# Kernel optimization log

Measured on AMD Instinct MI355X. Metric: run time of the kernel, lower is better.

The kernel has to match this reference:

```python
import jax, jax.numpy as jnp
import numpy as np

N, E = 40000, 640000
S_IN, V_IN = 64, 32            # input irreps: 64x0e + 32x1o (dim 160)
S_MID, V_MID = 96, 128         # tp output: (64+32)x0e, (64+32+32)x1o
S_OUT, V_OUT = 96, 32          # gate irreps_in: 64x0e scalars + 32x0e gates + 32x1o gated
R = 64                         # edge scalar (radial basis) dim
FC_HID = 64
W_NUMEL = 64 + 64 + 32 + 32 + 32  # per-edge tp weights ('uvu', v=1): 224
NUM_NEIGHBORS = 16.0


def setup_inputs() -> dict:
    key = jax.random.key(0)
    ks = jax.random.split(key, 13)
    return {
        "node_features": jax.random.normal(ks[0], (N, S_IN + 3 * V_IN), jnp.float32),
        "node_attr": jnp.ones((N, 1), jnp.float32),
        "edge_src": jax.random.randint(ks[1], (E,), 0, N),
        "edge_dst": jax.random.randint(ks[2], (E,), 0, N),
        "edge_attr": jax.random.normal(ks[3], (E, 4), jnp.float32),
        "edge_scalars": jax.random.normal(ks[4], (E, R), jnp.float32),
        "lin1_ws": jax.random.normal(ks[5], (S_IN, S_IN), jnp.float32),
        "lin1_wv": jax.random.normal(ks[6], (V_IN, V_IN), jnp.float32),
        "fc_w1": jax.random.normal(ks[7], (R, FC_HID), jnp.float32),
        "fc_w2": jax.random.normal(ks[8], (FC_HID, W_NUMEL), jnp.float32),
        "sc_ws": jax.random.normal(ks[9], (S_IN, S_OUT), jnp.float32),
        "sc_wv": jax.random.normal(ks[10], (V_IN, V_OUT), jnp.float32),
        "lin2_ws": jax.random.normal(ks[11], (S_MID, S_OUT), jnp.float32),
        "lin2_wv": jax.random.normal(ks[12], (V_MID, V_OUT), jnp.float32),
    }


def _inv(d):
    return 1.0 / jnp.sqrt(jnp.float32(d))


def _forward(node_features, node_attr, edge_attr, edge_scalars,
             lin1_ws, lin1_wv, fc_w1, fc_w2, sc_ws, sc_wv, lin2_ws, lin2_wv,
             edge_src, edge_dst):
    n = node_features.shape[0]
    s = node_features[:, :S_IN]                      # [N,64] 0e
    v = node_features[:, S_IN:].reshape(n, V_IN, 3)  # [N,32,3] 1o
    a = node_attr                                    # [N,1] scalar node attr

    # self-connection: FullyConnectedTensorProduct(input, 1x0e attr, out) == per-irrep linear
    sc_s = (s @ sc_ws) * a * _inv(S_IN)                                    # [N,96]
    sc_v = jnp.einsum('nci,cd->ndi', v, sc_wv) * a[:, :, None] * _inv(V_IN)  # [N,32,3]

    # lin1
    h_s = (s @ lin1_ws) * a * _inv(S_IN)
    h_v = jnp.einsum('nci,cd->ndi', v, lin1_wv) * a[:, :, None] * _inv(V_IN)

    # per-edge tensor-product weights from FC on edge scalars (silu MLP, no bias)
    hid = jax.nn.silu((edge_scalars @ fc_w1) * _inv(R))
    w = (hid @ fc_w2) * _inv(FC_HID)                 # [E,224]
    w1, w2, w3, w4, w5 = jnp.split(w, [64, 128, 160, 192], axis=-1)

    # gather source node features
    es = h_s[edge_src]                               # [E,64]
    ev = h_v[edge_src]                               # [E,32,3]
    e0 = edge_attr[:, :1]                            # [E,1]  0e
    e1 = edge_attr[:, 1:4]                           # [E,3]  1o

    # Clebsch-Gordan tensor product paths ('uvu', per-edge weights)
    m_s1 = w1 * es * e0                                                   # 0e x 0e -> 0e [E,64]
    m_s2 = w4 * jnp.einsum('eci,ei->ec', ev, e1) * _inv(3)                # 1o x 1o -> 0e [E,32]
    m_v1 = (w2 * es)[:, :, None] * e1[:, None, :]                         # 0e x 1o -> 1o [E,64,3]
    m_v2 = w3[:, :, None] * ev * e0[:, :, None]                           # 1o x 0e -> 1o [E,32,3]
    m_v3 = w5[:, :, None] * jnp.cross(ev, e1[:, None, :]) * _inv(2)       # 1o x 1o -> 1o [E,32,3]

    mid_s = jnp.concatenate([m_s1, m_s2], axis=-1)        # [E,96]
    mid_v = jnp.concatenate([m_v1, m_v2, m_v3], axis=1)   # [E,128,3]

    # scatter-sum to destination nodes, normalized by sqrt(num_neighbors)
    inv_nn = 1.0 / jnp.sqrt(jnp.float32(NUM_NEIGHBORS))
    agg_s = jax.ops.segment_sum(mid_s, edge_dst, num_segments=n) * inv_nn
    agg_v = jax.ops.segment_sum(mid_v, edge_dst, num_segments=n) * inv_nn

    # lin2
    o_s = (agg_s @ lin2_ws) * a * _inv(S_MID)                                  # [N,96]
    o_v = jnp.einsum('nci,cd->ndi', agg_v, lin2_wv) * a[:, :, None] * _inv(V_MID)  # [N,32,3]

    pre_s = sc_s + o_s
    pre_v = sc_v + o_v

    # Gate: silu on scalars, sigmoid gates multiply the l=1 features
    scalars = jax.nn.silu(pre_s[:, :64])
    gates = jax.nn.sigmoid(pre_s[:, 64:96])
    gated = gates[:, :, None] * pre_v                 # [N,32,3]
    return jnp.concatenate([scalars, gated.reshape(n, 3 * V_OUT)], axis=-1)  # [N,160]


def reference(node_features, node_attr, edge_src, edge_dst, edge_attr, edge_scalars,
              lin1_ws, lin1_wv, fc_w1, fc_w2, sc_ws, sc_wv, lin2_ws, lin2_wv):
    return _forward(node_features, node_attr, edge_attr, edge_scalars,
                    lin1_ws, lin1_wv, fc_w1, fc_w2, sc_ws, sc_wv, lin2_ws, lin2_wv,
                    edge_src, edge_dst)
```

## Files before the change

### kernel.cpp

```cpp
#include <hip/hip_runtime.h>

constexpr int N_NODES = 40000;
constexpr int N_EDGES = 640000;

constexpr float C_INV8     = 0.125f;
constexpr float C_INV_S32  = 0.17677669529663687f;
constexpr float C_INV_S3   = 0.57735026918962576f;
constexpr float C_INV_S2   = 0.70710678118654752f;
constexpr float C_INV_S96  = 0.10206207261596575f;
constexpr float C_INV_S128 = 0.08838834764831845f;
constexpr float C_INV_NN   = 0.25f;

typedef __attribute__((ext_vector_type(8))) short short8;
typedef __attribute__((ext_vector_type(4))) float f32x4;

__device__ __forceinline__ unsigned short f2bf(float x) {
  union { float f; unsigned int u; } v; v.f = x;
  unsigned int r = v.u + 0x7fffu + ((v.u >> 16) & 1u);
  return (unsigned short)(r >> 16);
}
__device__ __forceinline__ float bf2f(unsigned short h) {
  return __uint_as_float(((unsigned int)h) << 16);
}

__global__ __launch_bounds__(256) void k_prep(
    const float* __restrict__ fc_w1, const float* __restrict__ fc_w2,
    const float* __restrict__ lin2_ws, const float* __restrict__ lin2_wv,
    unsigned short* __restrict__ w1t, unsigned short* __restrict__ w2t,
    unsigned short* __restrict__ wst, unsigned short* __restrict__ wvt)
{
  int t = blockIdx.x * 256 + threadIdx.x;
  if (t < 4096) {
    int c = t >> 6, k = t & 63;
    w1t[c * 64 + k] = f2bf(fc_w1[k * 64 + c]);
  } else if (t < 4096 + 14336) {
    int u = t - 4096; int c = u >> 6, k = u & 63;
    w2t[c * 64 + k] = f2bf(fc_w2[k * 224 + c]);
  } else if (t < 18432 + 9216) {
    int u = t - 18432; int c = u / 96, k = u - c * 96;
    wst[c * 96 + k] = f2bf(lin2_ws[k * 96 + c]);
  } else if (t < 27648 + 4096) {
    int u = t - 27648; int d = u >> 7, k = u & 127;
    wvt[d * 128 + k] = f2bf(lin2_wv[k * 32 + d]);
  }
}

__global__ __launch_bounds__(256) void k_node_hs(
    const float* __restrict__ nf, const float* __restrict__ attr,
    const float* __restrict__ w, float* __restrict__ h_s)
{
  int t = blockIdx.x * 256 + threadIdx.x;
  if (t >= N_NODES * 64) return;
  int n = t >> 6, c = t & 63;
  const float* s = nf + (long)n * 160;
  float acc = 0.f;
  #pragma unroll 8
  for (int k = 0; k < 64; ++k) acc = fmaf(s[k], w[k * 64 + c], acc);
  h_s[t] = acc * attr[n] * C_INV8;
}

__global__ __launch_bounds__(256) void k_node_hv(
    const float* __restrict__ nf, const float* __restrict__ attr,
    const float* __restrict__ w, float* __restrict__ h_v)
{
  int t = blockIdx.x * 256 + threadIdx.x;
  if (t >= N_NODES * 32) return;
  int n = t >> 5, d = t & 31;
  const float* v = nf + (long)n * 160 + 64;
  float a0 = 0.f, a1 = 0.f, a2 = 0.f;
  #pragma unroll 8
  for (int c = 0; c < 32; ++c) {
    float wv = w[c * 32 + d];
    a0 = fmaf(v[3 * c + 0], wv, a0);
    a1 = fmaf(v[3 * c + 1], wv, a1);
    a2 = fmaf(v[3 * c + 2], wv, a2);
  }
  float sc = attr[n] * C_INV_S32;
  h_v[(long)t * 3 + 0] = a0 * sc;
  h_v[(long)t * 3 + 1] = a1 * sc;
  h_v[(long)t * 3 + 2] = a2 * sc;
}

__global__ __launch_bounds__(256, 2) void k_edge(
    const float* __restrict__ escal, const float* __restrict__ eattr,
    const int* __restrict__ esrc, const int* __restrict__ edst,
    const unsigned short* __restrict__ w1t, const unsigned short* __restrict__ w2t,
    const unsigned short* __restrict__ wst, const unsigned short* __restrict__ wvt,
    const float* __restrict__ h_s, const float* __restrict__ h_v,
    float* __restrict__ agg_s, float* __restrict__ agg_v)
{
  __shared__ unsigned short hid_lds[64 * 72];
  __shared__ unsigned short w_lds[64 * 232];
  int tid = threadIdx.x, warp = tid >> 6, lane = tid & 63;
  int lr = lane & 15, lg = lane >> 4;
  long e0 = (long)blockIdx.x * 64;
  int r0 = warp * 16;

  f32x4 acc[4] = {};
  #pragma unroll
  for (int ks = 0; ks < 2; ++ks) {
    const float* ap = escal + (e0 + r0 + lr) * 64 + ks * 32 + lg * 8;
    float4 a01 = *reinterpret_cast<const float4*>(ap);
    float4 a23 = *reinterpret_cast<const float4*>(ap + 4);
    short8 af;
    af[0] = (short)f2bf(a01.x); af[1] = (short)f2bf(a01.y);
    af[2] = (short)f2bf(a01.z); af[3] = (short)f2bf(a01.w);
    af[4] = (short)f2bf(a23.x); af[5] = (short)f2bf(a23.y);
    af[6] = (short)f2bf(a23.z); af[7] = (short)f2bf(a23.w);
    #pragma unroll
    for (int nt = 0; nt < 4; ++nt) {
      short8 bf = *reinterpret_cast<const short8*>(w1t + (nt * 16 + lr) * 64 + ks * 32 + lg * 8);
      acc[nt] = __builtin_amdgcn_mfma_f32_16x16x32_bf16(af, bf, acc[nt], 0, 0, 0);
    }
  }
  #pragma unroll
  for (int nt = 0; nt < 4; ++nt)
    #pragma unroll
    for (int r = 0; r < 4; ++r) {
      float x = acc[nt][r] * C_INV8;
      float h = x / (1.f + __expf(-x));
      hid_lds[(r0 + lg * 4 + r) * 72 + nt * 16 + lr] = f2bf(h);
    }
  __syncthreads();

  f32x4 acc2[14] = {};
  #pragma unroll
  for (int ks = 0; ks < 2; ++ks) {
    short8 af = *reinterpret_cast<const short8*>(hid_lds + (r0 + lr) * 72 + ks * 32 + lg * 8);
    #pragma unroll
    for (int nt = 0; nt < 14; ++nt) {
      short8 bf = *reinterpret_cast<const short8*>(w2t + (nt * 16 + lr) * 64 + ks * 32 + lg * 8);
      acc2[nt] = __builtin_amdgcn_mfma_f32_16x16x32_bf16(af, bf, acc2[nt], 0, 0, 0);
    }
  }
  #pragma unroll
  for (int nt = 0; nt < 14; ++nt)
    #pragma unroll
    for (int r = 0; r < 4; ++r)
      w_lds[(r0 + lg * 4 + r) * 232 + nt * 16 + lr] = f2bf(acc2[nt][r] * C_INV8);
  __syncthreads();

  long eM = e0 + r0 + lr;
  int srcM = esrc[eM];
  float ea0 = eattr[eM * 4 + 0];
  float e1x = eattr[eM * 4 + 1], e1y = eattr[eM * 4 + 2], e1z = eattr[eM * 4 + 3];

  float esv[16];
  {
    const float* hsr = h_s + (long)srcM * 64;
    *reinterpret_cast<float4*>(&esv[0])  = *reinterpret_cast<const float4*>(hsr + lg * 8);
    *reinterpret_cast<float4*>(&esv[4])  = *reinterpret_cast<const float4*>(hsr + lg * 8 + 4);
    *reinterpret_cast<float4*>(&esv[8])  = *reinterpret_cast<const float4*>(hsr + 32 + lg * 8);
    *reinterpret_cast<float4*>(&esv[12]) = *reinterpret_cast<const float4*>(hsr + 32 + lg * 8 + 4);
  }
  float evv[24];
  {
    const float* hvr = h_v + (long)srcM * 96 + lg * 24;
    #pragma unroll
    for (int q = 0; q < 6; ++q)
      *reinterpret_cast<float4*>(&evv[4 * q]) = *reinterpret_cast<const float4*>(hvr + 4 * q);
  }
  const unsigned short* wrow = w_lds + (r0 + lr) * 232;
  short8 w1a = *reinterpret_cast<const short8*>(wrow + lg * 8);
  short8 w1b = *reinterpret_cast<const short8*>(wrow + 32 + lg * 8);
  short8 w2a = *reinterpret_cast<const short8*>(wrow + 64 + lg * 8);
  short8 w2b = *reinterpret_cast<const short8*>(wrow + 96 + lg * 8);
  short8 w3s = *reinterpret_cast<const short8*>(wrow + 128 + lg * 8);
  short8 w4s = *reinterpret_cast<const short8*>(wrow + 160 + lg * 8);
  short8 w5s = *reinterpret_cast<const short8*>(wrow + 192 + lg * 8);

  f32x4 accS[6] = {};
  {
    short8 aS;
    #pragma unroll
    for (int j = 0; j < 8; ++j) aS[j] = (short)f2bf(bf2f((unsigned short)w1a[j]) * esv[j] * ea0);
    #pragma unroll
    for (int nt = 0; nt < 6; ++nt) {
      short8 b = *reinterpret_cast<const short8*>(wst + (nt * 16 + lr) * 96 + lg * 8);
      accS[nt] = __builtin_amdgcn_mfma_f32_16x16x32_bf16(aS, b, accS[nt], 0, 0, 0);
    }
    #pragma unroll
    for (int j = 0; j < 8; ++j) aS[j] = (short)f2bf(bf2f((unsigned short)w1b[j]) * esv[8 + j] * ea0);
    #pragma unroll
    for (int nt = 0; nt < 6; ++nt) {
      short8 b = *reinterpret_cast<const short8*>(wst + (nt * 16 + lr) * 96 + 32 + lg * 8);
      accS[nt] = __builtin_amdgcn_mfma_f32_16x16x32_bf16(aS, b, accS[nt], 0, 0, 0);
    }
    #pragma unroll
    for (int j = 0; j < 8; ++j) {
      float dot = evv[3 * j] * e1x + evv[3 * j + 1] * e1y + evv[3 * j + 2] * e1z;
      aS[j] = (short)f2bf(bf2f((unsigned short)w4s[j]) * dot * C_INV_S3);
    }
    #pragma unroll
    for (int nt = 0; nt < 6; ++nt) {
      short8 b = *reinterpret_cast<const short8*>(wst + (nt * 16 + lr) * 96 + 64 + lg * 8);
      accS[nt] = __builtin_amdgcn_mfma_f32_16x16x32_bf16(aS, b, accS[nt], 0, 0, 0);
    }
  }

  f32x4 accV[6] = {};
  #pragma unroll
  for (int i = 0; i < 3; ++i) {
    float e1i = (i == 0) ? e1x : (i == 1) ? e1y : e1z;
    short8 aV;
    #pragma unroll
    for (int j = 0; j < 8; ++j) aV[j] = (short)f2bf(bf2f((unsigned short)w2a[j]) * esv[j] * e1i);
    #pragma unroll
    for (int nt = 0; nt < 2; ++nt) {
      short8 b = *reinterpret_cast<const short8*>(wvt + (nt * 16 + lr) * 128 + lg * 8);
      accV[i * 2 + nt] = __builtin_amdgcn_mfma_f32_16x16x32_bf16(aV, b, accV[i * 2 + nt], 0, 0, 0);
    }
    #pragma unroll
    for (int j = 0; j < 8; ++j) aV[j] = (short)f2bf(bf2f((unsigned short)w2b[j]) * esv[8 + j] * e1i);
    #pragma unroll
    for (int nt = 0; nt < 2; ++nt) {
      short8 b = *reinterpret_cast<const short8*>(wvt + (nt * 16 + lr) * 128 + 32 + lg * 8);
      accV[i * 2 + nt] = __builtin_amdgcn_mfma_f32_16x16x32_bf16(aV, b, accV[i * 2 + nt], 0, 0, 0);
    }
    #pragma unroll
    for (int j = 0; j < 8; ++j) aV[j] = (short)f2bf(bf2f((unsigned short)w3s[j]) * evv[3 * j + i] * ea0);
    #pragma unroll
    for (int nt = 0; nt < 2; ++nt) {
      short8 b = *reinterpret_cast<const short8*>(wvt + (nt * 16 + lr) * 128 + 64 + lg * 8);
      accV[i * 2 + nt] = __builtin_amdgcn_mfma_f32_16x16x32_bf16(aV, b, accV[i * 2 + nt], 0, 0, 0);
    }
    #pragma unroll
    for (int j = 0; j < 8; ++j) {
      float ex = evv[3 * j], ey = evv[3 * j + 1], ez = evv[3 * j + 2];
      float cr = (i == 0) ? (ey * e1z - ez * e1y)
               : (i == 1) ? (ez * e1x - ex * e1z)
                          : (ex * e1y - ey * e1x);
      aV[j] = (short)f2bf(bf2f((unsigned short)w5s[j]) * cr * C_INV_S2);
    }
    #pragma unroll
    for (int nt = 0; nt < 2; ++nt) {
      short8 b = *reinterpret_cast<const short8*>(wvt + (nt * 16 + lr) * 128 + 96 + lg * 8);
      accV[i * 2 + nt] = __builtin_amdgcn_mfma_f32_16x16x32_bf16(aV, b, accV[i * 2 + nt], 0, 0, 0);
    }
  }

  #pragma unroll
  for (int r = 0; r < 4; ++r) {
    int dstR = edst[e0 + r0 + lg * 4 + r];
    float* asp = agg_s + (long)dstR * 96;
    #pragma unroll
    for (int nt = 0; nt < 6; ++nt) unsafeAtomicAdd(&asp[nt * 16 + lr], accS[nt][r]);
    float* avp = agg_v + (long)dstR * 96;
    #pragma unroll
    for (int q = 0; q < 6; ++q) {
      int i = q >> 1, nt = q & 1;
      unsafeAtomicAdd(&avp[i * 32 + nt * 16 + lr], accV[q][r]);
    }
  }
}

__global__ __launch_bounds__(256) void k_fin_s(
    const float* __restrict__ nf, const float* __restrict__ attr,
    const float* __restrict__ agg_s, const float* __restrict__ sc_ws,
    float* __restrict__ out, float* __restrict__ gate)
{
  int t = blockIdx.x * 256 + threadIdx.x;
  if (t >= N_NODES * 96) return;
  int n = t / 96, cch = t - n * 96;
  const float* s = nf + (long)n * 160;
  float acc2 = 0.f;
  #pragma unroll 8
  for (int k = 0; k < 64; ++k) acc2 = fmaf(s[k], sc_ws[k * 96 + cch], acc2);
  float pre = (agg_s[t] * (C_INV_NN * C_INV_S96) + acc2 * C_INV8) * attr[n];
  if (cch < 64) out[(long)n * 160 + cch] = pre / (1.f + __expf(-pre));
  else gate[n * 32 + cch - 64] = 1.f / (1.f + __expf(-pre));
}

__global__ __launch_bounds__(256) void k_fin_v(
    const float* __restrict__ nf, const float* __restrict__ attr,
    const float* __restrict__ agg_v, const float* __restrict__ sc_wv,
    const float* __restrict__ gate, float* __restrict__ out)
{
  int t = blockIdx.x * 256 + threadIdx.x;
  if (t >= N_NODES * 32) return;
  int n = t >> 5, d = t & 31;
  const float* v = nf + (long)n * 160 + 64;
  float s0 = 0.f, s1 = 0.f, s2 = 0.f;
  #pragma unroll 8
  for (int cc = 0; cc < 32; ++cc) {
    float wv = sc_wv[cc * 32 + d];
    s0 = fmaf(v[3 * cc + 0], wv, s0);
    s1 = fmaf(v[3 * cc + 1], wv, s1);
    s2 = fmaf(v[3 * cc + 2], wv, s2);
  }
  const float* ag = agg_v + (long)n * 96;
  float a = attr[n];
  float g = gate[t];
  float p0 = (ag[0 * 32 + d] * (C_INV_NN * C_INV_S128) + s0 * C_INV_S32) * a;
  float p1 = (ag[1 * 32 + d] * (C_INV_NN * C_INV_S128) + s1 * C_INV_S32) * a;
  float p2 = (ag[2 * 32 + d] * (C_INV_NN * C_INV_S128) + s2 * C_INV_S32) * a;
  float* o = out + (long)n * 160 + 64 + 3 * d;
  o[0] = g * p0; o[1] = g * p1; o[2] = g * p2;
}

extern "C" void kernel_launch(void* const* d_in, const int* in_sizes, int n_in,
                              void* d_out, int out_size, void* d_ws, size_t ws_size,
                              hipStream_t stream)
{
  const float* nf      = (const float*)d_in[0];
  const float* attr    = (const float*)d_in[1];
  const int*   esrc    = (const int*)d_in[2];
  const int*   edst    = (const int*)d_in[3];
  const float* eattr   = (const float*)d_in[4];
  const float* escal   = (const float*)d_in[5];
  const float* lin1_ws = (const float*)d_in[6];
  const float* lin1_wv = (const float*)d_in[7];
  const float* fc_w1   = (const float*)d_in[8];
  const float* fc_w2   = (const float*)d_in[9];
  const float* sc_ws   = (const float*)d_in[10];
  const float* sc_wv   = (const float*)d_in[11];
  const float* lin2_ws = (const float*)d_in[12];
  const float* lin2_wv = (const float*)d_in[13];
  float* out = (float*)d_out;

  float* ws    = (float*)d_ws;
  float* h_s   = ws;
  float* h_v   = h_s + (size_t)N_NODES * 64;
  float* agg_s = h_v + (size_t)N_NODES * 96;
  float* agg_v = agg_s + (size_t)N_NODES * 96;
  unsigned short* w1t = (unsigned short*)(agg_v + (size_t)N_NODES * 96);
  unsigned short* w2t = w1t + 64 * 64;
  unsigned short* wst = w2t + 224 * 64;
  unsigned short* wvt = wst + 96 * 96;
  float* gate = h_s;

  hipMemsetAsync(agg_s, 0, (size_t)N_NODES * 192 * sizeof(float), stream);
  k_prep<<<124, 256, 0, stream>>>(fc_w1, fc_w2, lin2_ws, lin2_wv, w1t, w2t, wst, wvt);
  k_node_hs<<<(N_NODES * 64 + 255) / 256, 256, 0, stream>>>(nf, attr, lin1_ws, h_s);
  k_node_hv<<<(N_NODES * 32 + 255) / 256, 256, 0, stream>>>(nf, attr, lin1_wv, h_v);
  k_edge<<<N_EDGES / 64, 256, 0, stream>>>(escal, eattr, esrc, edst,
                                           w1t, w2t, wst, wvt, h_s, h_v, agg_s, agg_v);
  k_fin_s<<<(N_NODES * 96 + 255) / 256, 256, 0, stream>>>(nf, attr, agg_s, sc_ws, out, gate);
  k_fin_v<<<(N_NODES * 32 + 255) / 256, 256, 0, stream>>>(nf, attr, agg_v, sc_wv, gate, out);
}
```

Before: 614.3 us.

## Replace atomic scatter with CSR-sorted gather aggregation of bf16 edge outputs

```diff
diff --git a/kernel.cpp b/kernel.cpp
--- a/kernel.cpp
+++ b/kernel.cpp
@@ -81,13 +81,64 @@
   h_v[(long)t * 3 + 2] = a2 * sc;
 }
 
-__global__ __launch_bounds__(256, 2) void k_edge(
+__global__ __launch_bounds__(256) void k_deg(const int* __restrict__ edst,
+                                             int* __restrict__ deg)
+{
+  int e = blockIdx.x * 256 + threadIdx.x;
+  if (e < N_EDGES) atomicAdd(&deg[edst[e]], 1);
+}
+
+__global__ __launch_bounds__(1024) void k_scan(const int* __restrict__ deg,
+                                               int* __restrict__ start,
+                                               int* __restrict__ cursor)
+{
+  __shared__ int psum[1024];
+  int tid = threadIdx.x;
+  const int PER = 40;
+  int base = tid * PER;
+  int s = 0;
+  for (int i = 0; i < PER; ++i) {
+    int idx = base + i;
+    if (idx < N_NODES) s += deg[idx];
+  }
+  psum[tid] = s;
+  __syncthreads();
+  for (int off = 1; off < 1024; off <<= 1) {
+    int v = psum[tid];
+    int u = (tid >= off) ? psum[tid - off] : 0;
+    __syncthreads();
+    psum[tid] = v + u;
+    __syncthreads();
+  }
+  int run = (tid == 0) ? 0 : psum[tid - 1];
+  for (int i = 0; i < PER; ++i) {
+    int idx = base + i;
+    if (idx < N_NODES) {
+      start[idx] = run; cursor[idx] = run;
+      run += deg[idx];
+    }
+  }
+  if (tid == 1023) start[N_NODES] = run;
+}
+
+__global__ __launch_bounds__(256) void k_fill(const int* __restrict__ edst,
+                                              int* __restrict__ cursor,
+                                              int* __restrict__ eid)
+{
+  int e = blockIdx.x * 256 + threadIdx.x;
+  if (e < N_EDGES) {
+    int p = atomicAdd(&cursor[edst[e]], 1);
+    eid[p] = e;
+  }
+}
+
+__global__ __launch_bounds__(256, 2) void k_edge2(
     const float* __restrict__ escal, const float* __restrict__ eattr,
-    const int* __restrict__ esrc, const int* __restrict__ edst,
+    const int* __restrict__ esrc,
     const unsigned short* __restrict__ w1t, const unsigned short* __restrict__ w2t,
     const unsigned short* __restrict__ wst, const unsigned short* __restrict__ wvt,
     const float* __restrict__ h_s, const float* __restrict__ h_v,
-    float* __restrict__ agg_s, float* __restrict__ agg_v)
+    unsigned short* __restrict__ e_out)
 {
   __shared__ unsigned short hid_lds[64 * 72];
   __shared__ unsigned short w_lds[64 * 232];
@@ -239,24 +290,217 @@
     }
   }
 
+  __syncthreads();
+  unsigned short* o_lds = w_lds;
+  #pragma unroll
+  for (int nt = 0; nt < 6; ++nt)
+    #pragma unroll
+    for (int r = 0; r < 4; ++r)
+      o_lds[(r0 + lg * 4 + r) * 200 + nt * 16 + lr] = f2bf(accS[nt][r]);
+  #pragma unroll
+  for (int q = 0; q < 6; ++q) {
+    int i = q >> 1, nt = q & 1;
+    #pragma unroll
+    for (int r = 0; r < 4; ++r)
+      o_lds[(r0 + lg * 4 + r) * 200 + 96 + i * 32 + nt * 16 + lr] = f2bf(accV[q][r]);
+  }
+  __syncthreads();
+
+  int row = tid >> 2, quad = tid & 3;
+  #pragma unroll
+  for (int c6 = 0; c6 < 6; ++c6) {
+    int cb = quad * 48 + c6 * 8;
+    float4 v4 = *reinterpret_cast<const float4*>(o_lds + row * 200 + cb);
+    *reinterpret_cast<float4*>(e_out + (e0 + row) * 192 + cb) = v4;
+  }
+}
+
+__global__ __launch_bounds__(256, 2) void k_edge_at(
+    const float* __restrict__ escal, const float* __restrict__ eattr,
+    const int* __restrict__ esrc, const int* __restrict__ edst,
+    const unsigned short* __restrict__ w1t, const unsigned short* __restrict__ w2t,
+    const unsigned short* __restrict__ wst, const unsigned short* __restrict__ wvt,
+    const float* __restrict__ h_s, const float* __restrict__ h_v,
+    float* __restrict__ agg)
+{
+  __shared__ unsigned short hid_lds[64 * 72];
+  __shared__ unsigned short w_lds[64 * 232];
+  int tid = threadIdx.x, warp = tid >> 6, lane = tid & 63;
+  int lr = lane & 15, lg = lane >> 4;
+  long e0 = (long)blockIdx.x * 64;
+  int r0 = warp * 16;
+
+  f32x4 acc[4] = {};
+  #pragma unroll
+  for (int ks = 0; ks < 2; ++ks) {
+    const float* ap = escal + (e0 + r0 + lr) * 64 + ks * 32 + lg * 8;
+    float4 a01 = *reinterpret_cast<const float4*>(ap);
+    float4 a23 = *reinterpret_cast<const float4*>(ap + 4);
+    short8 af;
+    af[0] = (short)f2bf(a01.x); af[1] = (short)f2bf(a01.y);
+    af[2] = (short)f2bf(a01.z); af[3] = (short)f2bf(a01.w);
+    af[4] = (short)f2bf(a23.x); af[5] = (short)f2bf(a23.y);
+    af[6] = (short)f2bf(a23.z); af[7] = (short)f2bf(a23.w);
+    #pragma unroll
+    for (int nt = 0; nt < 4; ++nt) {
+      short8 bf = *reinterpret_cast<const short8*>(w1t + (nt * 16 + lr) * 64 + ks * 32 + lg * 8);
+      acc[nt] = __builtin_amdgcn_mfma_f32_16x16x32_bf16(af, bf, acc[nt], 0, 0, 0);
+    }
+  }
+  #pragma unroll
+  for (int nt = 0; nt < 4; ++nt)
+    #pragma unroll
+    for (int r = 0; r < 4; ++r) {
+      float x = acc[nt][r] * C_INV8;
+      float h = x / (1.f + __expf(-x));
+      hid_lds[(r0 + lg * 4 + r) * 72 + nt * 16 + lr] = f2bf(h);
+    }
+  __syncthreads();
+
+  f32x4 acc2[14] = {};
+  #pragma unroll
+  for (int ks = 0; ks < 2; ++ks) {
+    short8 af = *reinterpret_cast<const short8*>(hid_lds + (r0 + lr) * 72 + ks * 32 + lg * 8);
+    #pragma unroll
+    for (int nt = 0; nt < 14; ++nt) {
+      short8 bf = *reinterpret_cast<const short8*>(w2t + (nt * 16 + lr) * 64 + ks * 32 + lg * 8);
+      acc2[nt] = __builtin_amdgcn_mfma_f32_16x16x32_bf16(af, bf, acc2[nt], 0, 0, 0);
+    }
+  }
+  #pragma unroll
+  for (int nt = 0; nt < 14; ++nt)
+    #pragma unroll
+    for (int r = 0; r < 4; ++r)
+      w_lds[(r0 + lg * 4 + r) * 232 + nt * 16 + lr] = f2bf(acc2[nt][r] * C_INV8);
+  __syncthreads();
+
+  long eM = e0 + r0 + lr;
+  int srcM = esrc[eM];
+  float ea0 = eattr[eM * 4 + 0];
+  float e1x = eattr[eM * 4 + 1], e1y = eattr[eM * 4 + 2], e1z = eattr[eM * 4 + 3];
+  float esv[16];
+  {
+    const float* hsr = h_s + (long)srcM * 64;
+    *reinterpret_cast<float4*>(&esv[0])  = *reinterpret_cast<const float4*>(hsr + lg * 8);
+    *reinterpret_cast<float4*>(&esv[4])  = *reinterpret_cast<const float4*>(hsr + lg * 8 + 4);
+    *reinterpret_cast<float4*>(&esv[8])  = *reinterpret_cast<const float4*>(hsr + 32 + lg * 8);
+    *reinterpret_cast<float4*>(&esv[12]) = *reinterpret_cast<const float4*>(hsr + 32 + lg * 8 + 4);
+  }
+  float evv[24];
+  {
+    const float* hvr = h_v + (long)srcM * 96 + lg * 24;
+    #pragma unroll
+    for (int q = 0; q < 6; ++q)
+      *reinterpret_cast<float4*>(&evv[4 * q]) = *reinterpret_cast<const float4*>(hvr + 4 * q);
+  }
+  const unsigned short* wrow = w_lds + (r0 + lr) * 232;
+  short8 w1a = *reinterpret_cast<const short8*>(wrow + lg * 8);
+  short8 w1b = *reinterpret_cast<const short8*>(wrow + 32 + lg * 8);
+  short8 w2a = *reinterpret_cast<const short8*>(wrow + 64 + lg * 8);
+  short8 w2b = *reinterpret_cast<const short8*>(wrow + 96 + lg * 8);
+  short8 w3s = *reinterpret_cast<const short8*>(wrow + 128 + lg * 8);
+  short8 w4s = *reinterpret_cast<const short8*>(wrow + 160 + lg * 8);
+  short8 w5s = *reinterpret_cast<const short8*>(wrow + 192 + lg * 8);
+
+  f32x4 accS[6] = {};
+  {
+    short8 aS;
+    #pragma unroll
+    for (int j = 0; j < 8; ++j) aS[j] = (short)f2bf(bf2f((unsigned short)w1a[j]) * esv[j] * ea0);
+    #pragma unroll
+    for (int nt = 0; nt < 6; ++nt) {
+      short8 b = *reinterpret_cast<const short8*>(wst + (nt * 16 + lr) * 96 + lg * 8);
+      accS[nt] = __builtin_amdgcn_mfma_f32_16x16x32_bf16(aS, b, accS[nt], 0, 0, 0);
+    }
+    #pragma unroll
+    for (int j = 0; j < 8; ++j) aS[j] = (short)f2bf(bf2f((unsigned short)w1b[j]) * esv[8 + j] * ea0);
+    #pragma unroll
+    for (int nt = 0; nt < 6; ++nt) {
+      short8 b = *reinterpret_cast<const short8*>(wst + (nt * 16 + lr) * 96 + 32 + lg * 8);
+      accS[nt] = __builtin_amdgcn_mfma_f32_16x16x32_bf16(aS, b, accS[nt], 0, 0, 0);
+    }
+    #pragma unroll
+    for (int j = 0; j < 8; ++j) {
+      float dot = evv[3 * j] * e1x + evv[3 * j + 1] * e1y + evv[3 * j + 2] * e1z;
+      aS[j] = (short)f2bf(bf2f((unsigned short)w4s[j]) * dot * C_INV_S3);
+    }
+    #pragma unroll
+    for (int nt = 0; nt < 6; ++nt) {
+      short8 b = *reinterpret_cast<const short8*>(wst + (nt * 16 + lr) * 96 + 64 + lg * 8);
+      accS[nt] = __builtin_amdgcn_mfma_f32_16x16x32_bf16(aS, b, accS[nt], 0, 0, 0);
+    }
+  }
+  f32x4 accV[6] = {};
+  #pragma unroll
+  for (int i = 0; i < 3; ++i) {
+    float e1i = (i == 0) ? e1x : (i == 1) ? e1y : e1z;
+    short8 aV;
+    #pragma unroll
+    for (int j = 0; j < 8; ++j) aV[j] = (short)f2bf(bf2f((unsigned short)w2a[j]) * esv[j] * e1i);
+    #pragma unroll
+    for (int nt = 0; nt < 2; ++nt) {
+      short8 b = *reinterpret_cast<const short8*>(wvt + (nt * 16 + lr) * 128 + lg * 8);
+      accV[i * 2 + nt] = __builtin_amdgcn_mfma_f32_16x16x32_bf16(aV, b, accV[i * 2 + nt], 0, 0, 0);
+    }
+    #pragma unroll
+    for (int j = 0; j < 8; ++j) aV[j] = (short)f2bf(bf2f((unsigned short)w2b[j]) * esv[8 + j] * e1i);
+    #pragma unroll
+    for (int nt = 0; nt < 2; ++nt) {
+      short8 b = *reinterpret_cast<const short8*>(wvt + (nt * 16 + lr) * 128 + 32 + lg * 8);
+      accV[i * 2 + nt] = __builtin_amdgcn_mfma_f32_16x16x32_bf16(aV, b, accV[i * 2 + nt], 0, 0, 0);
+    }
+    #pragma unroll
+    for (int j = 0; j < 8; ++j) aV[j] = (short)f2bf(bf2f((unsigned short)w3s[j]) * evv[3 * j + i] * ea0);
+    #pragma unroll
+    for (int nt = 0; nt < 2; ++nt) {
+      short8 b = *reinterpret_cast<const short8*>(wvt + (nt * 16 + lr) * 128 + 64 + lg * 8);
+      accV[i * 2 + nt] = __builtin_amdgcn_mfma_f32_16x16x32_bf16(aV, b, accV[i * 2 + nt], 0, 0, 0);
+    }
+    #pragma unroll
+    for (int j = 0; j < 8; ++j) {
+      float ex = evv[3 * j], ey = evv[3 * j + 1], ez = evv[3 * j + 2];
+      float cr = (i == 0) ? (ey * e1z - ez * e1y)
+               : (i == 1) ? (ez * e1x - ex * e1z)
+                          : (ex * e1y - ey * e1x);
+      aV[j] = (short)f2bf(bf2f((unsigned short)w5s[j]) * cr * C_INV_S2);
+    }
+    #pragma unroll
+    for (int nt = 0; nt < 2; ++nt) {
+      short8 b = *reinterpret_cast<const short8*>(wvt + (nt * 16 + lr) * 128 + 96 + lg * 8);
+      accV[i * 2 + nt] = __builtin_amdgcn_mfma_f32_16x16x32_bf16(aV, b, accV[i * 2 + nt], 0, 0, 0);
+    }
+  }
   #pragma unroll
   for (int r = 0; r < 4; ++r) {
     int dstR = edst[e0 + r0 + lg * 4 + r];
-    float* asp = agg_s + (long)dstR * 96;
-    #pragma unroll
-    for (int nt = 0; nt < 6; ++nt) unsafeAtomicAdd(&asp[nt * 16 + lr], accS[nt][r]);
-    float* avp = agg_v + (long)dstR * 96;
+    float* ap_ = agg + (long)dstR * 192;
+    #pragma unroll
+    for (int nt = 0; nt < 6; ++nt) unsafeAtomicAdd(&ap_[nt * 16 + lr], accS[nt][r]);
     #pragma unroll
     for (int q = 0; q < 6; ++q) {
       int i = q >> 1, nt = q & 1;
-      unsafeAtomicAdd(&avp[i * 32 + nt * 16 + lr], accV[q][r]);
-    }
-  }
+      unsafeAtomicAdd(&ap_[96 + i * 32 + nt * 16 + lr], accV[q][r]);
+    }
+  }
+}
+
+__global__ __launch_bounds__(192) void k_agg(
+    const int* __restrict__ start, const int* __restrict__ eid,
+    const unsigned short* __restrict__ eo, float* __restrict__ agg)
+{
+  int n = blockIdx.x, c = threadIdx.x;
+  int s0 = start[n], s1 = start[n + 1];
+  float acc = 0.f;
+  for (int k = s0; k < s1; ++k) {
+    int e = eid[k];
+    acc += bf2f(eo[(long)e * 192 + c]);
+  }
+  agg[(long)n * 192 + c] = acc;
 }
 
 __global__ __launch_bounds__(256) void k_fin_s(
     const float* __restrict__ nf, const float* __restrict__ attr,
-    const float* __restrict__ agg_s, const float* __restrict__ sc_ws,
+    const float* __restrict__ agg, const float* __restrict__ sc_ws,
     float* __restrict__ out, float* __restrict__ gate)
 {
   int t = blockIdx.x * 256 + threadIdx.x;
@@ -266,14 +510,14 @@
   float acc2 = 0.f;
   #pragma unroll 8
   for (int k = 0; k < 64; ++k) acc2 = fmaf(s[k], sc_ws[k * 96 + cch], acc2);
-  float pre = (agg_s[t] * (C_INV_NN * C_INV_S96) + acc2 * C_INV8) * attr[n];
+  float pre = (agg[(long)n * 192 + cch] * (C_INV_NN * C_INV_S96) + acc2 * C_INV8) * attr[n];
   if (cch < 64) out[(long)n * 160 + cch] = pre / (1.f + __expf(-pre));
   else gate[n * 32 + cch - 64] = 1.f / (1.f + __expf(-pre));
 }
 
 __global__ __launch_bounds__(256) void k_fin_v(
     const float* __restrict__ nf, const float* __restrict__ attr,
-    const float* __restrict__ agg_v, const float* __restrict__ sc_wv,
+    const float* __restrict__ agg, const float* __restrict__ sc_wv,
     const float* __restrict__ gate, float* __restrict__ out)
 {
   int t = blockIdx.x * 256 + threadIdx.x;
@@ -288,7 +532,7 @@
     s1 = fmaf(v[3 * cc + 1], wv, s1);
     s2 = fmaf(v[3 * cc + 2], wv, s2);
   }
-  const float* ag = agg_v + (long)n * 96;
+  const float* ag = agg + (long)n * 192 + 96;
   float a = attr[n];
   float g = gate[t];
   float p0 = (ag[0 * 32 + d] * (C_INV_NN * C_INV_S128) + s0 * C_INV_S32) * a;
@@ -308,33 +552,51 @@
   const int*   edst    = (const int*)d_in[3];
   const float* eattr   = (const float*)d_in[4];
   const float* escal   = (const float*)d_in[5];
-  const float* lin1_ws = (const float*)d_in[6];
-  const float* lin1_wv = (const float*)d_in[7];
   const float* fc_w1   = (const float*)d_in[8];
   const float* fc_w2   = (const float*)d_in[9];
   const float* sc_ws   = (const float*)d_in[10];
   const float* sc_wv   = (const float*)d_in[11];
+  const float* lin1_ws = (const float*)d_in[6];
+  const float* lin1_wv = (const float*)d_in[7];
   const float* lin2_ws = (const float*)d_in[12];
   const float* lin2_wv = (const float*)d_in[13];
   float* out = (float*)d_out;
 
-  float* ws    = (float*)d_ws;
-  float* h_s   = ws;
-  float* h_v   = h_s + (size_t)N_NODES * 64;
-  float* agg_s = h_v + (size_t)N_NODES * 96;
-  float* agg_v = agg_s + (size_t)N_NODES * 96;
-  unsigned short* w1t = (unsigned short*)(agg_v + (size_t)N_NODES * 96);
-  unsigned short* w2t = w1t + 64 * 64;
-  unsigned short* wst = w2t + 224 * 64;
-  unsigned short* wvt = wst + 96 * 96;
+  char* base = (char*)d_ws;
+  size_t off = 0;
+  auto carve = [&](size_t bytes) { void* p = base + off; off = (off + bytes + 63) & ~(size_t)63; return p; };
+  float* h_s   = (float*)carve((size_t)N_NODES * 64 * 4);
+  float* h_v   = (float*)carve((size_t)N_NODES * 96 * 4);
+  float* agg   = (float*)carve((size_t)N_NODES * 192 * 4);
+  unsigned short* w1t = (unsigned short*)carve(4096 * 2);
+  unsigned short* w2t = (unsigned short*)carve(14336 * 2);
+  unsigned short* wst = (unsigned short*)carve(9216 * 2);
+  unsigned short* wvt = (unsigned short*)carve(4096 * 2);
+  int* deg    = (int*)carve((size_t)N_NODES * 4);
+  int* startp = (int*)carve((size_t)(N_NODES + 1) * 4);
+  int* cursor = (int*)carve((size_t)N_NODES * 4);
+  int* eid    = (int*)carve((size_t)N_EDGES * 4);
+  unsigned short* e_out = (unsigned short*)carve((size_t)N_EDGES * 192 * 2);
+  bool csr = (off <= ws_size);
   float* gate = h_s;
 
-  hipMemsetAsync(agg_s, 0, (size_t)N_NODES * 192 * sizeof(float), stream);
   k_prep<<<124, 256, 0, stream>>>(fc_w1, fc_w2, lin2_ws, lin2_wv, w1t, w2t, wst, wvt);
   k_node_hs<<<(N_NODES * 64 + 255) / 256, 256, 0, stream>>>(nf, attr, lin1_ws, h_s);
   k_node_hv<<<(N_NODES * 32 + 255) / 256, 256, 0, stream>>>(nf, attr, lin1_wv, h_v);
-  k_edge<<<N_EDGES / 64, 256, 0, stream>>>(escal, eattr, esrc, edst,
-                                           w1t, w2t, wst, wvt, h_s, h_v, agg_s, agg_v);
-  k_fin_s<<<(N_NODES * 96 + 255) / 256, 256, 0, stream>>>(nf, attr, agg_s, sc_ws, out, gate);
-  k_fin_v<<<(N_NODES * 32 + 255) / 256, 256, 0, stream>>>(nf, attr, agg_v, sc_wv, gate, out);
-}
+
+  if (csr) {
+    hipMemsetAsync(deg, 0, (size_t)N_NODES * 4, stream);
+    k_deg<<<(N_EDGES + 255) / 256, 256, 0, stream>>>(edst, deg);
+    k_scan<<<1, 1024, 0, stream>>>(deg, startp, cursor);
+    k_fill<<<(N_EDGES + 255) / 256, 256, 0, stream>>>(edst, cursor, eid);
+    k_edge2<<<N_EDGES / 64, 256, 0, stream>>>(escal, eattr, esrc,
+                                              w1t, w2t, wst, wvt, h_s, h_v, e_out);
+    k_agg<<<N_NODES, 192, 0, stream>>>(startp, eid, e_out, agg);
+  } else {
+    hipMemsetAsync(agg, 0, (size_t)N_NODES * 192 * 4, stream);
+    k_edge_at<<<N_EDGES / 64, 256, 0, stream>>>(escal, eattr, esrc, edst,
+                                                w1t, w2t, wst, wvt, h_s, h_v, agg);
+  }
+  k_fin_s<<<(N_NODES * 96 + 255) / 256, 256, 0, stream>>>(nf, attr, agg, sc_ws, out, gate);
+  k_fin_v<<<(N_NODES * 32 + 255) / 256, 256, 0, stream>>>(nf, attr, agg, sc_wv, gate, out);
+}
```

Result: slower. 818.0 us (+33.2%).

## Replace scatter atomics with CSR-sorted gather aggregation via bf16 per-edge buffer

Applied to the files above, without the earlier changes.

```diff
diff --git a/kernel.cpp b/kernel.cpp
--- a/kernel.cpp
+++ b/kernel.cpp
@@ -15,9 +15,8 @@
 typedef __attribute__((ext_vector_type(4))) float f32x4;
 
 __device__ __forceinline__ unsigned short f2bf(float x) {
-  union { float f; unsigned int u; } v; v.f = x;
-  unsigned int r = v.u + 0x7fffu + ((v.u >> 16) & 1u);
-  return (unsigned short)(r >> 16);
+  __bf16 b = (__bf16)x;
+  return __builtin_bit_cast(unsigned short, b);
 }
 __device__ __forceinline__ float bf2f(unsigned short h) {
   return __uint_as_float(((unsigned int)h) << 16);
@@ -38,10 +37,10 @@
     w2t[c * 64 + k] = f2bf(fc_w2[k * 224 + c]);
   } else if (t < 18432 + 9216) {
     int u = t - 18432; int c = u / 96, k = u - c * 96;
-    wst[c * 96 + k] = f2bf(lin2_ws[k * 96 + c]);
+    wst[c * 96 + k] = f2bf(lin2_ws[k * 96 + c] * (C_INV_NN * C_INV_S96));
   } else if (t < 27648 + 4096) {
     int u = t - 27648; int d = u >> 7, k = u & 127;
-    wvt[d * 128 + k] = f2bf(lin2_wv[k * 32 + d]);
+    wvt[d * 128 + k] = f2bf(lin2_wv[k * 32 + d] * (C_INV_NN * C_INV_S128));
   }
 }
 
@@ -81,13 +80,64 @@
   h_v[(long)t * 3 + 2] = a2 * sc;
 }
 
-__global__ __launch_bounds__(256, 2) void k_edge(
+__global__ __launch_bounds__(256) void k_deg(const int* __restrict__ edst,
+                                             int* __restrict__ deg)
+{
+  int e = blockIdx.x * 256 + threadIdx.x;
+  if (e < N_EDGES) atomicAdd(&deg[edst[e]], 1);
+}
+
+__global__ __launch_bounds__(1024) void k_scan(const int* __restrict__ deg,
+                                               int* __restrict__ start,
+                                               int* __restrict__ cursor)
+{
+  __shared__ int psum[1024];
+  int tid = threadIdx.x;
+  const int PER = 40;
+  int base = tid * PER;
+  int s = 0;
+  for (int i = 0; i < PER; ++i) {
+    int idx = base + i;
+    if (idx < N_NODES) s += deg[idx];
+  }
+  psum[tid] = s;
+  __syncthreads();
+  for (int off = 1; off < 1024; off <<= 1) {
+    int v = psum[tid];
+    int u = (tid >= off) ? psum[tid - off] : 0;
+    __syncthreads();
+    psum[tid] = v + u;
+    __syncthreads();
+  }
+  int run = (tid == 0) ? 0 : psum[tid - 1];
+  for (int i = 0; i < PER; ++i) {
+    int idx = base + i;
+    if (idx < N_NODES) {
+      start[idx] = run; cursor[idx] = run;
+      run += deg[idx];
+    }
+  }
+  if (tid == 1023) start[N_NODES] = run;
+}
+
+__global__ __launch_bounds__(256) void k_fill(const int* __restrict__ edst,
+                                              int* __restrict__ cursor,
+                                              int* __restrict__ eid)
+{
+  int e = blockIdx.x * 256 + threadIdx.x;
+  if (e < N_EDGES) {
+    int p = atomicAdd(&cursor[edst[e]], 1);
+    eid[p] = e;
+  }
+}
+
+__global__ __launch_bounds__(256, 2) void k_edge2(
     const float* __restrict__ escal, const float* __restrict__ eattr,
-    const int* __restrict__ esrc, const int* __restrict__ edst,
+    const int* __restrict__ esrc,
     const unsigned short* __restrict__ w1t, const unsigned short* __restrict__ w2t,
     const unsigned short* __restrict__ wst, const unsigned short* __restrict__ wvt,
     const float* __restrict__ h_s, const float* __restrict__ h_v,
-    float* __restrict__ agg_s, float* __restrict__ agg_v)
+    unsigned short* __restrict__ e_out)
 {
   __shared__ unsigned short hid_lds[64 * 72];
   __shared__ unsigned short w_lds[64 * 232];
@@ -95,6 +145,26 @@
   int lr = lane & 15, lg = lane >> 4;
   long e0 = (long)blockIdx.x * 64;
   int r0 = warp * 16;
+
+  long eM = e0 + r0 + lr;
+  int srcM = esrc[eM];
+  float4 ea4 = *reinterpret_cast<const float4*>(eattr + eM * 4);
+  float ea0 = ea4.x, e1x = ea4.y, e1y = ea4.z, e1z = ea4.w;
+  float esv[16];
+  {
+    const float* hsr = h_s + (long)srcM * 64;
+    *reinterpret_cast<float4*>(&esv[0])  = *reinterpret_cast<const float4*>(hsr + lg * 8);
+    *reinterpret_cast<float4*>(&esv[4])  = *reinterpret_cast<const float4*>(hsr + lg * 8 + 4);
+    *reinterpret_cast<float4*>(&esv[8])  = *reinterpret_cast<const float4*>(hsr + 32 + lg * 8);
+    *reinterpret_cast<float4*>(&esv[12]) = *reinterpret_cast<const float4*>(hsr + 32 + lg * 8 + 4);
+  }
+  float evv[24];
+  {
+    const float* hvr = h_v + (long)srcM * 96 + lg * 24;
+    #pragma unroll
+    for (int q = 0; q < 6; ++q)
+      *reinterpret_cast<float4*>(&evv[4 * q]) = *reinterpret_cast<const float4*>(hvr + 4 * q);
+  }
 
   f32x4 acc[4] = {};
   #pragma unroll
@@ -121,7 +191,6 @@
       float h = x / (1.f + __expf(-x));
       hid_lds[(r0 + lg * 4 + r) * 72 + nt * 16 + lr] = f2bf(h);
     }
-  __syncthreads();
 
   f32x4 acc2[14] = {};
   #pragma unroll
@@ -138,28 +207,7 @@
     #pragma unroll
     for (int r = 0; r < 4; ++r)
       w_lds[(r0 + lg * 4 + r) * 232 + nt * 16 + lr] = f2bf(acc2[nt][r] * C_INV8);
-  __syncthreads();
-
-  long eM = e0 + r0 + lr;
-  int srcM = esrc[eM];
-  float ea0 = eattr[eM * 4 + 0];
-  float e1x = eattr[eM * 4 + 1], e1y = eattr[eM * 4 + 2], e1z = eattr[eM * 4 + 3];
-
-  float esv[16];
-  {
-    const float* hsr = h_s + (long)srcM * 64;
-    *reinterpret_cast<float4*>(&esv[0])  = *reinterpret_cast<const float4*>(hsr + lg * 8);
-    *reinterpret_cast<float4*>(&esv[4])  = *reinterpret_cast<const float4*>(hsr + lg * 8 + 4);
-    *reinterpret_cast<float4*>(&esv[8])  = *reinterpret_cast<const float4*>(hsr + 32 + lg * 8);
-    *reinterpret_cast<float4*>(&esv[12]) = *reinterpret_cast<const float4*>(hsr + 32 + lg * 8 + 4);
-  }
-  float evv[24];
-  {
-    const float* hvr = h_v + (long)srcM * 96 + lg * 24;
-    #pragma unroll
-    for (int q = 0; q < 6; ++q)
-      *reinterpret_cast<float4*>(&evv[4 * q]) = *reinterpret_cast<const float4*>(hvr + 4 * q);
-  }
+
   const unsigned short* wrow = w_lds + (r0 + lr) * 232;
   short8 w1a = *reinterpret_cast<const short8*>(wrow + lg * 8);
   short8 w1b = *reinterpret_cast<const short8*>(wrow + 32 + lg * 8);
@@ -239,24 +287,60 @@
     }
   }
 
-  #pragma unroll
-  for (int r = 0; r < 4; ++r) {
-    int dstR = edst[e0 + r0 + lg * 4 + r];
-    float* asp = agg_s + (long)dstR * 96;
-    #pragma unroll
-    for (int nt = 0; nt < 6; ++nt) unsafeAtomicAdd(&asp[nt * 16 + lr], accS[nt][r]);
-    float* avp = agg_v + (long)dstR * 96;
-    #pragma unroll
-    for (int q = 0; q < 6; ++q) {
-      int i = q >> 1, nt = q & 1;
-      unsafeAtomicAdd(&avp[i * 32 + nt * 16 + lr], accV[q][r]);
-    }
-  }
+  unsigned short* o_lds = w_lds;
+  #pragma unroll
+  for (int nt = 0; nt < 6; ++nt)
+    #pragma unroll
+    for (int r = 0; r < 4; ++r)
+      o_lds[(r0 + lg * 4 + r) * 232 + nt * 16 + lr] = f2bf(accS[nt][r]);
+  #pragma unroll
+  for (int q = 0; q < 6; ++q) {
+    int i = q >> 1, nt = q & 1;
+    #pragma unroll
+    for (int r = 0; r < 4; ++r)
+      o_lds[(r0 + lg * 4 + r) * 232 + 96 + i * 32 + nt * 16 + lr] = f2bf(accV[q][r]);
+  }
+
+  #pragma unroll
+  for (int c3 = 0; c3 < 6; ++c3) {
+    int chunk = c3 * 64 + lane;
+    int row = chunk / 24, col = chunk % 24;
+    float4 v4 = *reinterpret_cast<const float4*>(o_lds + (r0 + row) * 232 + col * 8);
+    *reinterpret_cast<float4*>(e_out + (e0 + r0 + row) * 192 + col * 8) = v4;
+  }
+}
+
+__global__ __launch_bounds__(128) void k_agg(
+    const int* __restrict__ start, const int* __restrict__ eid,
+    const unsigned short* __restrict__ eo, float* __restrict__ agg)
+{
+  int n = blockIdx.x, tid = threadIdx.x;
+  if (tid >= 96) return;
+  int s0 = start[n], s1 = start[n + 1];
+  float acc0 = 0.f, acc1 = 0.f;
+  for (int base = s0; base < s1; base += 16) {
+    int cnt = s1 - base; if (cnt > 16) cnt = 16;
+    unsigned int vals[16];
+    #pragma unroll
+    for (int k = 0; k < 16; ++k) {
+      int idx = base + k; if (idx > s1 - 1) idx = s1 - 1;
+      int e = eid[idx];
+      unsigned int v = *reinterpret_cast<const unsigned int*>(eo + (long)e * 192 + tid * 2);
+      vals[k] = (k < cnt) ? v : 0u;
+    }
+    #pragma unroll
+    for (int k = 0; k < 16; ++k) {
+      acc0 += bf2f((unsigned short)(vals[k] & 0xffffu));
+      acc1 += bf2f((unsigned short)(vals[k] >> 16));
+    }
+  }
+  float2 o = make_float2(acc0, acc1);
+  *reinterpret_cast<float2*>(agg + (long)n * 192 + tid * 2) = o;
 }
 
 __global__ __launch_bounds__(256) void k_fin_s(
     const float* __restrict__ nf, const float* __restrict__ attr,
-    const float* __restrict__ agg_s, const float* __restrict__ sc_ws,
+    const float* __restrict__ agg, const float* __restrict__ sc_ws,
     float* __restrict__ out, float* __restrict__ gate)
 {
   int t = blockIdx.x * 256 + threadIdx.x;
@@ -266,14 +350,14 @@
   float acc2 = 0.f;
   #pragma unroll 8
   for (int k = 0; k < 64; ++k) acc2 = fmaf(s[k], sc_ws[k * 96 + cch], acc2);
-  float pre = (agg_s[t] * (C_INV_NN * C_INV_S96) + acc2 * C_INV8) * attr[n];
+  float pre = (agg[(long)n * 192 + cch] + acc2 * C_INV8) * attr[n];
   if (cch < 64) out[(long)n * 160 + cch] = pre / (1.f + __expf(-pre));
   else gate[n * 32 + cch - 64] = 1.f / (1.f + __expf(-pre));
 }
 
 __global__ __launch_bounds__(256) void k_fin_v(
     const float* __restrict__ nf, const float* __restrict__ attr,
-    const float* __restrict__ agg_v, const float* __restrict__ sc_wv,
+    const float* __restrict__ agg, const float* __restrict__ sc_wv,
     const float* __restrict__ gate, float* __restrict__ out)
 {
   int t = blockIdx.x * 256 + threadIdx.x;
@@ -288,12 +372,12 @@
     s1 = fmaf(v[3 * cc + 1], wv, s1);
     s2 = fmaf(v[3 * cc + 2], wv, s2);
   }
-  const float* ag = agg_v + (long)n * 96;
+  const float* ag = agg + (long)n * 192 + 96;
   float a = attr[n];
   float g = gate[t];
-  float p0 = (ag[0 * 32 + d] * (C_INV_NN * C_INV_S128) + s0 * C_INV_S32) * a;
-  float p1 = (ag[1 * 32 + d] * (C_INV_NN * C_INV_S128) + s1 * C_INV_S32) * a;
-  float p2 = (ag[2 * 32 + d] * (C_INV_NN * C_INV_S128) + s2 * C_INV_S32) * a;
+  float p0 = (ag[0 * 32 + d] + s0 * C_INV_S32) * a;
+  float p1 = (ag[1 * 32 + d] + s1 * C_INV_S32) * a;
+  float p2 = (ag[2 * 32 + d] + s2 * C_INV_S32) * a;
   float* o = out + (long)n * 160 + 64 + 3 * d;
   o[0] = g * p0; o[1] = g * p1; o[2] = g * p2;
 }
@@ -318,23 +402,34 @@
   const float* lin2_wv = (const float*)d_in[13];
   float* out = (float*)d_out;
 
-  float* ws    = (float*)d_ws;
-  float* h_s   = ws;
-  float* h_v   = h_s + (size_t)N_NODES * 64;
-  float* agg_s = h_v + (size_t)N_NODES * 96;
-  float* agg_v = agg_s + (size_t)N_NODES * 96;
-  unsigned short* w1t = (unsigned short*)(agg_v + (size_t)N_NODES * 96);
-  unsigned short* w2t = w1t + 64 * 64;
-  unsigned short* wst = w2t + 224 * 64;
-  unsigned short* wvt = wst + 96 * 96;
+  char* base = (char*)d_ws;
+  size_t off = 0;
+  auto carve = [&](size_t bytes) { void* p = base + off; off = (off + bytes + 63) & ~(size_t)63; return p; };
+  float* h_s   = (float*)carve((size_t)N_NODES * 64 * 4);
+  float* h_v   = (float*)carve((size_t)N_NODES * 96 * 4);
+  float* agg   = (float*)carve((size_t)N_NODES * 192 * 4);
+  unsigned short* w1t = (unsigned short*)carve(4096 * 2);
+  unsigned short* w2t = (unsigned short*)carve(14336 * 2);
+  unsigned short* wst = (unsigned short*)carve(9216 * 2);
+  unsigned short* wvt = (unsigned short*)carve(4096 * 2);
+  int* deg    = (int*)carve((size_t)N_NODES * 4);
+  int* startp = (int*)carve((size_t)(N_NODES + 1) * 4);
+  int* cursor = (int*)carve((size_t)N_NODES * 4);
+  int* eid    = (int*)carve((size_t)N_EDGES * 4);
+  unsigned short* e_out = (unsigned short*)carve((size_t)N_EDGES * 192 * 2);
   float* gate = h_s;
 
-  hipMemsetAsync(agg_s, 0, (size_t)N_NODES * 192 * sizeof(float), stream);
   k_prep<<<124, 256, 0, stream>>>(fc_w1, fc_w2, lin2_ws, lin2_wv, w1t, w2t, wst, wvt);
   k_node_hs<<<(N_NODES * 64 + 255) / 256, 256, 0, stream>>>(nf, attr, lin1_ws, h_s);
   k_node_hv<<<(N_NODES * 32 + 255) / 256, 256, 0, stream>>>(nf, attr, lin1_wv, h_v);
-  k_edge<<<N_EDGES / 64, 256, 0, stream>>>(escal, eattr, esrc, edst,
-                                           w1t, w2t, wst, wvt, h_s, h_v, agg_s, agg_v);
-  k_fin_s<<<(N_NODES * 96 + 255) / 256, 256, 0, stream>>>(nf, attr, agg_s, sc_ws, out, gate);
-  k_fin_v<<<(N_NODES * 32 + 255) / 256, 256, 0, stream>>>(nf, attr, agg_v, sc_wv, gate, out);
-}
+
+  hipMemsetAsync(deg, 0, (size_t)N_NODES * 4, stream);
+  k_deg<<<(N_EDGES + 255) / 256, 256, 0, stream>>>(edst, deg);
+  k_scan<<<1, 1024, 0, stream>>>(deg, startp, cursor);
+  k_fill<<<(N_EDGES + 255) / 256, 256, 0, stream>>>(edst, cursor, eid);
+  k_edge2<<<N_EDGES / 64, 256, 0, stream>>>(escal, eattr, esrc,
+                                            w1t, w2t, wst, wvt, h_s, h_v, e_out);
+  k_agg<<<N_NODES, 128, 0, stream>>>(startp, eid, e_out, agg);
+  k_fin_s<<<(N_NODES * 96 + 255) / 256, 256, 0, stream>>>(nf, attr, agg, sc_ws, out, gate);
+  k_fin_v<<<(N_NODES * 32 + 255) / 256, 256, 0, stream>>>(nf, attr, agg, sc_wv, gate, out);
+}
```

After: 704.6 us. 14.7% more time.
